# Kernel optimization log

Measured on AMD Instinct MI355X. Metric: run time of the kernel, lower is better.

The kernel has to match this reference:

```python
import jax, jax.numpy as jnp
import numpy as np

DIM = 768
HEADS = 12
HEAD_DIM = DIM // HEADS
SCALE = HEAD_DIM ** -0.5
B = 8
N = 2121   # 1 cls + 1600 + 400 + 100 + 20 text
NT = 20

# token ranges: cls [0,1), x0 [1,1601), x1 [1601,2001), x2 [2001,2101), t [2101,2121)
SLICES = {'cls': (0, 1), 'x0': (1, 1601), 'x1': (1601, 2001), 'x2': (2001, 2101), 't': (2101, 2121)}


def setup_inputs() -> dict:
    key = jax.random.key(0)
    k1, k2, k3, k4 = jax.random.split(key, 4)
    src = jax.random.normal(k1, (B, N, DIM), dtype=jnp.float32)
    visu_mask = jnp.zeros((B, 2101), dtype=bool)   # True = masked out
    text_mask = jnp.zeros((B, NT), dtype=bool)
    w_qkv = jax.random.normal(k2, (DIM, 3 * DIM), dtype=jnp.float32) * 0.02
    w_proj = jax.random.normal(k3, (DIM, DIM), dtype=jnp.float32) * 0.02
    b_proj = jax.random.normal(k4, (DIM,), dtype=jnp.float32) * 0.02
    return {'src': src, 'visu_mask': visu_mask, 'text_mask': text_mask,
            'w_qkv': w_qkv, 'w_proj': w_proj, 'b_proj': b_proj}


def _attn(q, k, v, mask):
    # q: [B,H,Nq,D], k/v: [B,H,Nk,D], mask: [B,Nk] bool (True = masked)
    scores = jnp.einsum('bhqd,bhkd->bhqk', q * SCALE, k)
    scores = jnp.where(mask[:, None, None, :], -jnp.inf, scores)
    p = jax.nn.softmax(scores, axis=-1)
    o = jnp.einsum('bhqk,bhkd->bhqd', p, v)          # [B,H,Nq,D]
    return o.transpose(0, 2, 1, 3).reshape(q.shape[0], q.shape[2], -1)  # [B,Nq,C]


def reference(src, visu_mask, text_mask, w_qkv, w_proj, b_proj):
    qkv = (src @ w_qkv).reshape(B, N, 3, HEADS, HEAD_DIM).transpose(2, 0, 3, 1, 4)
    q, k, v = qkv[0], qkv[1], qkv[2]                  # [B,H,N,D]

    def blk(t, lo, hi):
        return t[:, :, lo:hi, :]

    (c0, c1), (a0, a1), (b0, b1), (d0, d1), (t0, t1) = (
        SLICES['cls'], SLICES['x0'], SLICES['x1'], SLICES['x2'], SLICES['t'])

    x0_mask = visu_mask[:, a0:a1]
    x1_mask = visu_mask[:, b0:b1]
    x2_mask = visu_mask[:, d0:d1]
    full_mask = jnp.concatenate([visu_mask, text_mask], axis=1)   # [B, N]

    # cls attends to everything
    cls = _attn(blk(q, c0, c1), k, v, full_mask)
    # x2 attends to x0+x1+x2+t
    k_x2 = jnp.concatenate([blk(k, a0, a1), blk(k, b0, b1), blk(k, d0, d1), blk(k, t0, t1)], axis=2)
    v_x2 = jnp.concatenate([blk(v, a0, a1), blk(v, b0, b1), blk(v, d0, d1), blk(v, t0, t1)], axis=2)
    m_x2 = jnp.concatenate([x0_mask, x1_mask, x2_mask, text_mask], axis=1)
    x2 = _attn(blk(q, d0, d1), k_x2, v_x2, m_x2)
    # x1 attends to x0+x1+t
    k_x1 = jnp.concatenate([blk(k, a0, a1), blk(k, b0, b1), blk(k, t0, t1)], axis=2)
    v_x1 = jnp.concatenate([blk(v, a0, a1), blk(v, b0, b1), blk(v, t0, t1)], axis=2)
    m_x1 = jnp.concatenate([x0_mask, x1_mask, text_mask], axis=1)
    x1 = _attn(blk(q, b0, b1), k_x1, v_x1, m_x1)
    # x0 attends to x0+t
    k_x0 = jnp.concatenate([blk(k, a0, a1), blk(k, t0, t1)], axis=2)
    v_x0 = jnp.concatenate([blk(v, a0, a1), blk(v, t0, t1)], axis=2)
    m_x0 = jnp.concatenate([x0_mask, text_mask], axis=1)
    x0 = _attn(blk(q, a0, a1), k_x0, v_x0, m_x0)
    # text attends to everything
    t = _attn(blk(q, t0, t1), k, v, full_mask)

    x = jnp.concatenate([cls, x0, x1, x2, t], axis=1)
    return x @ w_proj + b_proj
```

## Files before the change

### kernel.cpp

```cpp
#include <hip/hip_runtime.h>
#include <stdint.h>

typedef short           bf16x8 __attribute__((ext_vector_type(8)));
typedef float           f32x4  __attribute__((ext_vector_type(4)));
typedef float           f32x16 __attribute__((ext_vector_type(16)));
typedef unsigned short  u16;
typedef u16             u16x8  __attribute__((ext_vector_type(8)));
typedef uint32_t        u32;

#define NB    8
#define NSEQ  2121
#define NPAD  2176
#define MROWS 16968
#define MPAD  17024
#define NH    12

#if __has_builtin(__builtin_amdgcn_exp2f)
#define EXP2F(x) __builtin_amdgcn_exp2f(x)
#else
#define EXP2F(x) exp2f(x)
#endif

#define MASK_BIAS   (-30000.0f)
#define INVALID_S   (-90000.0f)

__device__ __forceinline__ u16 f2bf(float f) {
  uint32_t u = __float_as_uint(f);
  u += 0x7fffu + ((u >> 16) & 1u);
  return (u16)(u >> 16);
}

__global__ void transpose_cast(const float* __restrict__ in, u16* __restrict__ out,
                               int R, int C, int scale_cols, float scale)
{
  __shared__ float tile[32][33];
  const int c0 = blockIdx.x * 32, r0 = blockIdx.y * 32;
  const int tx = threadIdx.x, ty = threadIdx.y;
#pragma unroll
  for (int i = 0; i < 4; i++) {
    const int r = r0 + ty + i * 8;
    tile[ty + i * 8][tx] = in[(size_t)r * C + c0 + tx];
  }
  __syncthreads();
#pragma unroll
  for (int i = 0; i < 4; i++) {
    const int c = c0 + ty + i * 8;
    float v = tile[tx][ty + i * 8];
    if (c < scale_cols) v *= scale;
    out[(size_t)c * R + r0 + tx] = f2bf(v);
  }
}

__global__ __launch_bounds__(256) void gemm_qkv_kernel(
    const float* __restrict__ src, const u16* __restrict__ wt,
    u16* __restrict__ qk, u16* __restrict__ vt)
{
  __shared__ u16 As[128][40];
  __shared__ u16 Bs[128][40];
  const int tid  = threadIdx.x;
  const int lane = tid & 63, wave = tid >> 6;
  const int wr = wave >> 1, wc = wave & 1;
  const int col = lane & 15, grp = lane >> 4;
  const int m0 = blockIdx.y * 128, n0 = blockIdx.x * 128;
  const int arow = tid >> 1, akoff = (tid & 1) * 16;

  const f32x4 fz = {0.f, 0.f, 0.f, 0.f};
  f32x4 acc[4][4];
#pragma unroll
  for (int i = 0; i < 4; i++)
#pragma unroll
    for (int j = 0; j < 4; j++) acc[i][j] = fz;

  const int m = m0 + arow;
  const bool mv = m < MROWS;
  const float4* sbase = (const float4*)(src + (size_t)m * 768 + akoff);
  const u16*   bbase  = wt + (size_t)(n0 + arow) * 768 + akoff;

  float4 a0 = {0,0,0,0}, a1 = {0,0,0,0}, a2 = {0,0,0,0}, a3 = {0,0,0,0};
  u16x8 bb0, bb1;
  if (mv) { a0 = sbase[0]; a1 = sbase[1]; a2 = sbase[2]; a3 = sbase[3]; }
  bb0 = *(const u16x8*)(bbase);
  bb1 = *(const u16x8*)(bbase + 8);

  for (int kb = 0; kb < 768; kb += 32) {
    u16x8 t0, t1;
    t0[0] = f2bf(a0.x); t0[1] = f2bf(a0.y); t0[2] = f2bf(a0.z); t0[3] = f2bf(a0.w);
    t0[4] = f2bf(a1.x); t0[5] = f2bf(a1.y); t0[6] = f2bf(a1.z); t0[7] = f2bf(a1.w);
    t1[0] = f2bf(a2.x); t1[1] = f2bf(a2.y); t1[2] = f2bf(a2.z); t1[3] = f2bf(a2.w);
    t1[4] = f2bf(a3.x); t1[5] = f2bf(a3.y); t1[6] = f2bf(a3.z); t1[7] = f2bf(a3.w);
    *(u16x8*)&As[arow][akoff]     = t0;
    *(u16x8*)&As[arow][akoff + 8] = t1;
    *(u16x8*)&Bs[arow][akoff]     = bb0;
    *(u16x8*)&Bs[arow][akoff + 8] = bb1;
    __syncthreads();

    if (kb + 32 < 768) {
      const int o = (kb + 32) >> 2;
      if (mv) { a0 = sbase[o]; a1 = sbase[o + 1]; a2 = sbase[o + 2]; a3 = sbase[o + 3]; }
      bb0 = *(const u16x8*)(bbase + kb + 32);
      bb1 = *(const u16x8*)(bbase + kb + 40);
    }

    bf16x8 af[4], bfr[4];
#pragma unroll
    for (int mt = 0; mt < 4; mt++) af[mt]  = *(const bf16x8*)&As[wr * 64 + mt * 16 + col][grp * 8];
#pragma unroll
    for (int nt = 0; nt < 4; nt++) bfr[nt] = *(const bf16x8*)&Bs[wc * 64 + nt * 16 + col][grp * 8];
#pragma unroll
    for (int mt = 0; mt < 4; mt++)
#pragma unroll
      for (int nt = 0; nt < 4; nt++)
        acc[mt][nt] = __builtin_amdgcn_mfma_f32_16x16x32_bf16(af[mt], bfr[nt], acc[mt][nt], 0, 0, 0);
    __syncthreads();
  }

#pragma unroll
  for (int mt = 0; mt < 4; mt++) {
#pragma unroll
    for (int r = 0; r < 4; r++) {
      const int mm = m0 + wr * 64 + mt * 16 + grp * 4 + r;
      if (mm >= MROWS) continue;
      const uint32_t bb = (uint32_t)mm / 2121u;
      const uint32_t nn = (uint32_t)mm - bb * 2121u;
#pragma unroll
      for (int nt = 0; nt < 4; nt++) {
        const int c = n0 + wc * 64 + nt * 16 + col;
        const u16 bits = f2bf(acc[mt][nt][r]);
        if (c < 1536) {
          qk[(size_t)mm * 1536 + c] = bits;
        } else {
          const int hd = c - 1536;
          const int h = hd >> 6, d = hd & 63;
          vt[((size_t)(bb * NH + h) * 64 + d) * NPAD + nn] = bits;
        }
      }
    }
  }
}

__global__ __launch_bounds__(256) void gemm_proj_kernel(
    const u16* __restrict__ A, const u16* __restrict__ Bt,
    const float* __restrict__ bias, float* __restrict__ out)
{
  __shared__ u16 As[128][40];
  __shared__ u16 Bs[128][40];
  const int tid  = threadIdx.x;
  const int lane = tid & 63, wave = tid >> 6;
  const int wr = wave >> 1, wc = wave & 1;
  const int col = lane & 15, grp = lane >> 4;
  const int m0 = blockIdx.y * 128, n0 = blockIdx.x * 128;
  const int arow = tid >> 1, akoff = (tid & 1) * 16;

  const f32x4 fz = {0.f, 0.f, 0.f, 0.f};
  f32x4 acc[4][4];
#pragma unroll
  for (int i = 0; i < 4; i++)
#pragma unroll
    for (int j = 0; j < 4; j++) acc[i][j] = fz;

  const u16* abase = A  + (size_t)(m0 + arow) * 768 + akoff;
  const u16* bbase = Bt + (size_t)(n0 + arow) * 768 + akoff;
  u16x8 aa0, aa1, bb0, bb1;
  aa0 = *(const u16x8*)(abase);
  aa1 = *(const u16x8*)(abase + 8);
  bb0 = *(const u16x8*)(bbase);
  bb1 = *(const u16x8*)(bbase + 8);

  for (int kb = 0; kb < 768; kb += 32) {
    *(u16x8*)&As[arow][akoff]     = aa0;
    *(u16x8*)&As[arow][akoff + 8] = aa1;
    *(u16x8*)&Bs[arow][akoff]     = bb0;
    *(u16x8*)&Bs[arow][akoff + 8] = bb1;
    __syncthreads();

    if (kb + 32 < 768) {
      aa0 = *(const u16x8*)(abase + kb + 32);
      aa1 = *(const u16x8*)(abase + kb + 40);
      bb0 = *(const u16x8*)(bbase + kb + 32);
      bb1 = *(const u16x8*)(bbase + kb + 40);
    }

    bf16x8 af[4], bfr[4];
#pragma unroll
    for (int mt = 0; mt < 4; mt++) af[mt]  = *(const bf16x8*)&As[wr * 64 + mt * 16 + col][grp * 8];
#pragma unroll
    for (int nt = 0; nt < 4; nt++) bfr[nt] = *(const bf16x8*)&Bs[wc * 64 + nt * 16 + col][grp * 8];
#pragma unroll
    for (int mt = 0; mt < 4; mt++)
#pragma unroll
      for (int nt = 0; nt < 4; nt++)
        acc[mt][nt] = __builtin_amdgcn_mfma_f32_16x16x32_bf16(af[mt], bfr[nt], acc[mt][nt], 0, 0, 0);
    __syncthreads();
  }

#pragma unroll
  for (int mt = 0; mt < 4; mt++) {
#pragma unroll
    for (int r = 0; r < 4; r++) {
      const int mm = m0 + wr * 64 + mt * 16 + grp * 4 + r;
      if (mm >= MROWS) continue;
#pragma unroll
      for (int nt = 0; nt < 4; nt++) {
        const int c = n0 + wc * 64 + nt * 16 + col;
        out[(size_t)mm * 768 + c] = acc[mt][nt][r] + bias[c];
      }
    }
  }
}

__global__ __launch_bounds__(256) void attn_kernel(
    const u16* __restrict__ qkbuf, const u16* __restrict__ vt,
    const unsigned char* __restrict__ visu, const unsigned char* __restrict__ text,
    u16* __restrict__ attnout)
{
  __shared__ __align__(16) u16 Ks[2][64][72];
  __shared__ __align__(16) u16 Vs[2][64][72];
  __shared__ __align__(16) float biasAll[NPAD];
  __shared__ __align__(16) float lduf[4][32];
  __shared__ u32 tileflags[34];

  const int tid  = threadIdx.x;
  const int lane = tid & 63, wave = tid >> 6;
  const int l31 = lane & 31, h = lane >> 5;

  const int fid = blockIdx.x;
  const int swz = (fid & 7) * 204 + (fid >> 3);
  const int qtile = swz % 17;
  const int bh = swz / 17;
  const int b = bh / NH, hh = bh % NH;
  const int qt0 = qtile * 128;
  const int q0 = qt0 + wave * 32;
  const int qrow = q0 + l31;

  for (int i = tid; i < NPAD; i += 256) {
    float bb = MASK_BIAS;
    if (i < 2101)      bb = visu[b * 2101 + i] ? MASK_BIAS : 0.0f;
    else if (i < 2121) bb = text[b * 20 + (i - 2101)] ? MASK_BIAS : 0.0f;
    biasAll[i] = bb;
  }
  if (tid < 34) tileflags[tid] = 0u;
  __syncthreads();
  if (tid < 136) {
    const int t = tid >> 2;
    const float* p = &biasAll[t * 64 + (tid & 3) * 16];
    float s = 0.f;
#pragma unroll
    for (int j = 0; j < 16; j++) s += p[j];
    if (s != 0.f) atomicOr(&tileflags[t], 1u);
  }

  bf16x8 qf[4];
  {
    const u16* qp = qkbuf + (size_t)(b * NSEQ + qrow) * 1536 + hh * 64 + h * 8;
#pragma unroll
    for (int s = 0; s < 4; s++) qf[s] = *(const bf16x8*)(qp + s * 16);
  }

  int ks, ke, ex;
  if (qrow == 0)        { ks = 0; ke = 2121; ex = 0; }
  else if (qrow < 1601) { ks = 1; ke = 1601; ex = 1; }
  else if (qrow < 2001) { ks = 1; ke = 2001; ex = 1; }
  else if (qrow < 2101) { ks = 1; ke = 2121; ex = 0; }
  else if (qrow < 2121) { ks = 0; ke = 2121; ex = 0; }
  else                  { ks = 0; ke = 0;    ex = 0; }

  const int hi = (qt0 + 127 < 2120) ? (qt0 + 127) : 2120;
  int ke_tile, extra;
  if (qt0 == 0 || hi >= 2001) { ke_tile = 2121; extra = 0; }
  else if (hi >= 1601)        { ke_tile = 2001; extra = 1; }
  else                        { ke_tile = 1601; extra = 1; }
  const int nkv = (ke_tile + 63) >> 6;
  const int ntot = nkv + extra;

  f32x16 O0, O1;
#pragma unroll
  for (int i = 0; i < 16; i++) { O0[i] = 0.f; O1[i] = 0.f; }
  float lrun = 0.f;

  const int srow = tid >> 2, skoff = (tid & 3) * 16;
  const size_t vbase = (size_t)(b * NH + hh) * 64 * NPAD;
  const u16* kbase = qkbuf + (size_t)(b * NSEQ + srow) * 1536 + 768 + hh * 64 + skoff;
  const u16* vrow  = vt + vbase + (size_t)srow * NPAD + skoff;

  {
    u16x8 k0 = *(const u16x8*)kbase;
    u16x8 k1 = *(const u16x8*)(kbase + 8);
    u16x8 v0 = *(const u16x8*)vrow;
    u16x8 v1 = *(const u16x8*)(vrow + 8);
    *(u16x8*)&Ks[0][srow][skoff]     = k0;
    *(u16x8*)&Ks[0][srow][skoff + 8] = k1;
    *(u16x8*)&Vs[0][srow][skoff]     = v0;
    *(u16x8*)&Vs[0][srow][skoff + 8] = v1;
  }
  __syncthreads();

  u16x8 kpre0, kpre1, vpre0, vpre1;

  for (int it = 0; it < ntot; ++it) {
    const int cur = it & 1;
    const int kv0 = (it < nkv) ? it * 64 : 2096;
    const bool more = (it + 1 < ntot);

    if (more) {
      const int kvn = (it + 1 < nkv) ? (it + 1) * 64 : 2096;
      const u16* kp = kbase + (size_t)kvn * 1536;
      kpre0 = *(const u16x8*)kp;
      kpre1 = *(const u16x8*)(kp + 8);
      const u16* vp = vrow + kvn;
      vpre0 = *(const u16x8*)vp;
      vpre1 = *(const u16x8*)(vp + 8);
    }

    const int skipl = (kv0 >= ke) && !((ex != 0) && (kv0 < 2121) && (kv0 + 64 > 2101));
    if (!__all(skipl)) {
      f32x16 S0, S1;
#pragma unroll
      for (int i = 0; i < 16; i++) { S0[i] = 0.f; S1[i] = 0.f; }
      __builtin_amdgcn_s_setprio(1);
#pragma unroll
      for (int s = 0; s < 4; s++) {
        const bf16x8 k0 = *(const bf16x8*)&Ks[cur][l31][s * 16 + h * 8];
        const bf16x8 k1 = *(const bf16x8*)&Ks[cur][32 + l31][s * 16 + h * 8];
        S0 = __builtin_amdgcn_mfma_f32_32x32x16_bf16(k0, qf[s], S0, 0, 0, 0);
        S1 = __builtin_amdgcn_mfma_f32_32x32x16_bf16(k1, qf[s], S1, 0, 0, 0);
      }
      __builtin_amdgcn_s_setprio(0);

      const int fastl = (kv0 >= ks) && (kv0 + 64 <= ke);
      const bool tf = (it < nkv) ? (tileflags[it] != 0u) : true;
      const bool plain = __all(fastl) && !tf;
      if (!plain) {
#pragma unroll
        for (int m = 0; m < 4; m++) {
          const f32x4 b0 = *(const f32x4*)&biasAll[kv0 + 8 * m + 4 * h];
          const f32x4 b1 = *(const f32x4*)&biasAll[kv0 + 32 + 8 * m + 4 * h];
#pragma unroll
          for (int r = 0; r < 4; r++) {
            {
              const int key = kv0 + 8 * m + 4 * h + r;
              const bool valid = ((key >= ks) && (key < ke)) ||
                                 ((ex != 0) && (key >= 2101) && (key < 2121));
              const float sv = S0[4 * m + r] + b0[r];
              S0[4 * m + r] = valid ? sv : INVALID_S;
            }
            {
              const int key = kv0 + 32 + 8 * m + 4 * h + r;
              const bool valid = ((key >= ks) && (key < ke)) ||
                                 ((ex != 0) && (key >= 2101) && (key < 2121));
              const float sv = S1[4 * m + r] + b1[r];
              S1[4 * m + r] = valid ? sv : INVALID_S;
            }
          }
        }
      }

      float ls = 0.f;
#pragma unroll
      for (int i = 0; i < 16; i++) { const float p = EXP2F(S0[i]); S0[i] = p; ls += p; }
#pragma unroll
      for (int i = 0; i < 16; i++) { const float p = EXP2F(S1[i]); S1[i] = p; ls += p; }
      lrun += ls;

      bf16x8 pa[4];
      {
        u32 w[8];
#pragma unroll
        for (int j = 0; j < 8; j++) {
          u32 t;
          asm("v_cvt_pk_bf16_f32 %0, %1, %2" : "=v"(t) : "v"(S0[2 * j]), "v"(S0[2 * j + 1]));
          w[j] = t;
        }
        asm("v_permlane32_swap_b32 %0, %1" : "+v"(w[0]), "+v"(w[2]));
        asm("v_permlane32_swap_b32 %0, %1" : "+v"(w[1]), "+v"(w[3]));
        asm("v_permlane32_swap_b32 %0, %1" : "+v"(w[4]), "+v"(w[6]));
        asm("v_permlane32_swap_b32 %0, %1" : "+v"(w[5]), "+v"(w[7]));
        union { u32 u[4]; bf16x8 v; } f0, f1;
        f0.u[0] = w[0]; f0.u[1] = w[1]; f0.u[2] = w[2]; f0.u[3] = w[3];
        f1.u[0] = w[4]; f1.u[1] = w[5]; f1.u[2] = w[6]; f1.u[3] = w[7];
        pa[0] = f0.v; pa[1] = f1.v;
      }
      {
        u32 w[8];
#pragma unroll
        for (int j = 0; j < 8; j++) {
          u32 t;
          asm("v_cvt_pk_bf16_f32 %0, %1, %2" : "=v"(t) : "v"(S1[2 * j]), "v"(S1[2 * j + 1]));
          w[j] = t;
        }
        asm("v_permlane32_swap_b32 %0, %1" : "+v"(w[0]), "+v"(w[2]));
        asm("v_permlane32_swap_b32 %0, %1" : "+v"(w[1]), "+v"(w[3]));
        asm("v_permlane32_swap_b32 %0, %1" : "+v"(w[4]), "+v"(w[6]));
        asm("v_permlane32_swap_b32 %0, %1" : "+v"(w[5]), "+v"(w[7]));
        union { u32 u[4]; bf16x8 v; } f0, f1;
        f0.u[0] = w[0]; f0.u[1] = w[1]; f0.u[2] = w[2]; f0.u[3] = w[3];
        f1.u[0] = w[4]; f1.u[1] = w[5]; f1.u[2] = w[6]; f1.u[3] = w[7];
        pa[2] = f0.v; pa[3] = f1.v;
      }

      __builtin_amdgcn_s_setprio(1);
#pragma unroll
      for (int ck = 0; ck < 4; ck++) {
        const bf16x8 vf0 = *(const bf16x8*)&Vs[cur][l31][ck * 16 + h * 8];
        const bf16x8 vf1 = *(const bf16x8*)&Vs[cur][32 + l31][ck * 16 + h * 8];
        O0 = __builtin_amdgcn_mfma_f32_32x32x16_bf16(pa[ck], vf0, O0, 0, 0, 0);
        O1 = __builtin_amdgcn_mfma_f32_32x32x16_bf16(pa[ck], vf1, O1, 0, 0, 0);
      }
      __builtin_amdgcn_s_setprio(0);
    }

    if (more) {
      *(u16x8*)&Ks[cur ^ 1][srow][skoff]     = kpre0;
      *(u16x8*)&Ks[cur ^ 1][srow][skoff + 8] = kpre1;
      *(u16x8*)&Vs[cur ^ 1][srow][skoff]     = vpre0;
      *(u16x8*)&Vs[cur ^ 1][srow][skoff + 8] = vpre1;
    }
    __syncthreads();
  }

  float ltot = lrun + __shfl_xor(lrun, 32);
  if (h == 0) lduf[wave][l31] = ltot;
#pragma unroll
  for (int m = 0; m < 4; m++) {
    const f32x4 lv = *(const f32x4*)&lduf[wave][8 * m + 4 * h];
#pragma unroll
    for (int r = 0; r < 4; r++) {
      const float linv = (lv[r] > 0.f) ? 1.0f / lv[r] : 0.f;
      const int n = q0 + 8 * m + 4 * h + r;
      if (n >= NSEQ) continue;
      u16* op = attnout + (size_t)(b * NSEQ + n) * 768 + hh * 64 + l31;
      op[0]  = f2bf(O0[4 * m + r] * linv);
      op[32] = f2bf(O1[4 * m + r] * linv);
    }
  }
}

extern "C" void kernel_launch(void* const* d_in, const int* in_sizes, int n_in,
                              void* d_out, int out_size, void* d_ws, size_t ws_size,
                              hipStream_t stream) {
  const float* src  = (const float*)d_in[0];
  const unsigned char* visu = (const unsigned char*)d_in[1];
  const unsigned char* text = (const unsigned char*)d_in[2];
  const float* w_qkv = (const float*)d_in[3];
  const float* w_proj = (const float*)d_in[4];
  const float* b_proj = (const float*)d_in[5];
  float* out = (float*)d_out;

  char* ws = (char*)d_ws;
  size_t off = 0;
  auto alloc = [&](size_t bytes) { char* p = ws + off; off += (bytes + 255) & ~(size_t)255; return p; };
  u16* wqkv_t  = (u16*)alloc((size_t)2304 * 768 * 2);
  u16* wproj_t = (u16*)alloc((size_t)768 * 768 * 2);
  u16* qk      = (u16*)alloc((size_t)MPAD * 1536 * 2);
  u16* vtb     = (u16*)alloc((size_t)NB * NH * 64 * NPAD * 2);
  u16* attnb   = (u16*)alloc((size_t)MPAD * 768 * 2);
  (void)ws_size; (void)in_sizes; (void)n_in; (void)out_size;

  transpose_cast<<<dim3(2304 / 32, 768 / 32), dim3(32, 8), 0, stream>>>(w_qkv, wqkv_t, 768, 2304, 768, 0.125f * 1.4426950408889634f);
  transpose_cast<<<dim3(768 / 32, 768 / 32), dim3(32, 8), 0, stream>>>(w_proj, wproj_t, 768, 768, 0, 1.0f);
  gemm_qkv_kernel<<<dim3(18, 133), dim3(256), 0, stream>>>(src, wqkv_t, qk, vtb);
  attn_kernel<<<dim3(1632), dim3(256), 0, stream>>>(qk, vtb, visu, text, attnb);
  gemm_proj_kernel<<<dim3(6, 133), dim3(256), 0, stream>>>(attnb, wproj_t, b_proj, out);
}
```

Before: 408.7 us.

## Precast src to bf16, widen attention tiles to 256 queries, bitmask key masks

A separate kernel casts src to bf16 once, so the QKV GEMM loads bf16 directly instead of converting fp32 inside the K loop. The attention kernel goes to 512 threads with 256-query tiles, so each K/V tile loaded into shared memory is reused by twice as many query rows. The per-key float bias array and tile flags are replaced by 64-bit ballot bitmasks, and the bf16 src buffer is reused as the attention output. The extra cast kernel adds a full read and write of src, and the larger blocks cut the grid from 1632 to 864 blocks, which may reduce occupancy and load balance.

Result: faster. 391.8 us (-4.1%).

```diff
diff --git a/kernel.cpp b/kernel.cpp
--- a/kernel.cpp
+++ b/kernel.cpp
@@ -7,6 +7,7 @@
 typedef unsigned short  u16;
 typedef u16             u16x8  __attribute__((ext_vector_type(8)));
 typedef uint32_t        u32;
+typedef unsigned long long u64;
 
 #define NB    8
 #define NSEQ  2121
@@ -21,7 +22,6 @@
 #define EXP2F(x) exp2f(x)
 #endif
 
-#define MASK_BIAS   (-30000.0f)
 #define INVALID_S   (-90000.0f)
 
 __device__ __forceinline__ u16 f2bf(float f) {
@@ -51,8 +51,20 @@
   }
 }
 
+__global__ __launch_bounds__(256) void cast_src_bf16(const float* __restrict__ in,
+                                                     u16* __restrict__ out)
+{
+  const size_t i = ((size_t)blockIdx.x * 256 + threadIdx.x) * 8;
+  float4 a = *(const float4*)(in + i);
+  float4 b = *(const float4*)(in + i + 4);
+  u16x8 t;
+  t[0] = f2bf(a.x); t[1] = f2bf(a.y); t[2] = f2bf(a.z); t[3] = f2bf(a.w);
+  t[4] = f2bf(b.x); t[5] = f2bf(b.y); t[6] = f2bf(b.z); t[7] = f2bf(b.w);
+  *(u16x8*)(out + i) = t;
+}
+
 __global__ __launch_bounds__(256) void gemm_qkv_kernel(
-    const float* __restrict__ src, const u16* __restrict__ wt,
+    const u16* __restrict__ srcb, const u16* __restrict__ wt,
     u16* __restrict__ qk, u16* __restrict__ vt)
 {
   __shared__ u16 As[128][40];
@@ -71,32 +83,24 @@
 #pragma unroll
     for (int j = 0; j < 4; j++) acc[i][j] = fz;
 
-  const int m = m0 + arow;
-  const bool mv = m < MROWS;
-  const float4* sbase = (const float4*)(src + (size_t)m * 768 + akoff);
-  const u16*   bbase  = wt + (size_t)(n0 + arow) * 768 + akoff;
-
-  float4 a0 = {0,0,0,0}, a1 = {0,0,0,0}, a2 = {0,0,0,0}, a3 = {0,0,0,0};
-  u16x8 bb0, bb1;
-  if (mv) { a0 = sbase[0]; a1 = sbase[1]; a2 = sbase[2]; a3 = sbase[3]; }
+  const u16* abase = srcb + (size_t)(m0 + arow) * 768 + akoff;
+  const u16* bbase = wt   + (size_t)(n0 + arow) * 768 + akoff;
+  u16x8 aa0, aa1, bb0, bb1;
+  aa0 = *(const u16x8*)(abase);
+  aa1 = *(const u16x8*)(abase + 8);
   bb0 = *(const u16x8*)(bbase);
   bb1 = *(const u16x8*)(bbase + 8);
 
   for (int kb = 0; kb < 768; kb += 32) {
-    u16x8 t0, t1;
-    t0[0] = f2bf(a0.x); t0[1] = f2bf(a0.y); t0[2] = f2bf(a0.z); t0[3] = f2bf(a0.w);
-    t0[4] = f2bf(a1.x); t0[5] = f2bf(a1.y); t0[6] = f2bf(a1.z); t0[7] = f2bf(a1.w);
-    t1[0] = f2bf(a2.x); t1[1] = f2bf(a2.y); t1[2] = f2bf(a2.z); t1[3] = f2bf(a2.w);
-    t1[4] = f2bf(a3.x); t1[5] = f2bf(a3.y); t1[6] = f2bf(a3.z); t1[7] = f2bf(a3.w);
-    *(u16x8*)&As[arow][akoff]     = t0;
-    *(u16x8*)&As[arow][akoff + 8] = t1;
+    *(u16x8*)&As[arow][akoff]     = aa0;
+    *(u16x8*)&As[arow][akoff + 8] = aa1;
     *(u16x8*)&Bs[arow][akoff]     = bb0;
     *(u16x8*)&Bs[arow][akoff + 8] = bb1;
     __syncthreads();
 
     if (kb + 32 < 768) {
-      const int o = (kb + 32) >> 2;
-      if (mv) { a0 = sbase[o]; a1 = sbase[o + 1]; a2 = sbase[o + 2]; a3 = sbase[o + 3]; }
+      aa0 = *(const u16x8*)(abase + kb + 32);
+      aa1 = *(const u16x8*)(abase + kb + 40);
       bb0 = *(const u16x8*)(bbase + kb + 32);
       bb1 = *(const u16x8*)(bbase + kb + 40);
     }
@@ -208,50 +212,42 @@
   }
 }
 
-__global__ __launch_bounds__(256) void attn_kernel(
+__global__ __launch_bounds__(512) void attn_kernel(
     const u16* __restrict__ qkbuf, const u16* __restrict__ vt,
     const unsigned char* __restrict__ visu, const unsigned char* __restrict__ text,
     u16* __restrict__ attnout)
 {
   __shared__ __align__(16) u16 Ks[2][64][72];
   __shared__ __align__(16) u16 Vs[2][64][72];
-  __shared__ __align__(16) float biasAll[NPAD];
-  __shared__ __align__(16) float lduf[4][32];
-  __shared__ u32 tileflags[34];
+  __shared__ __align__(16) u64 mb64[34];
+  __shared__ __align__(16) float lduf[8][32];
 
   const int tid  = threadIdx.x;
   const int lane = tid & 63, wave = tid >> 6;
   const int l31 = lane & 31, h = lane >> 5;
 
   const int fid = blockIdx.x;
-  const int swz = (fid & 7) * 204 + (fid >> 3);
-  const int qtile = swz % 17;
-  const int bh = swz / 17;
+  const int swz = (fid & 7) * 108 + (fid >> 3);
+  const int qtile = swz % 9;
+  const int bh = swz / 9;
   const int b = bh / NH, hh = bh % NH;
-  const int qt0 = qtile * 128;
+  const int qt0 = qtile * 256;
   const int q0 = qt0 + wave * 32;
   const int qrow = q0 + l31;
 
-  for (int i = tid; i < NPAD; i += 256) {
-    float bb = MASK_BIAS;
-    if (i < 2101)      bb = visu[b * 2101 + i] ? MASK_BIAS : 0.0f;
-    else if (i < 2121) bb = text[b * 20 + (i - 2101)] ? MASK_BIAS : 0.0f;
-    biasAll[i] = bb;
-  }
-  if (tid < 34) tileflags[tid] = 0u;
-  __syncthreads();
-  if (tid < 136) {
-    const int t = tid >> 2;
-    const float* p = &biasAll[t * 64 + (tid & 3) * 16];
-    float s = 0.f;
-#pragma unroll
-    for (int j = 0; j < 16; j++) s += p[j];
-    if (s != 0.f) atomicOr(&tileflags[t], 1u);
-  }
-
+  for (int c = wave; c < 34; c += 8) {
+    const int key = c * 64 + lane;
+    int mb = 1;
+    if (key < 2101)      mb = visu[b * 2101 + key] ? 1 : 0;
+    else if (key < 2121) mb = text[b * 20 + (key - 2101)] ? 1 : 0;
+    const u64 bal = __ballot(mb != 0);
+    if (lane == 0) mb64[c] = bal;
+  }
+
+  const int qload = (qrow < NSEQ) ? qrow : (NSEQ - 1);
   bf16x8 qf[4];
   {
-    const u16* qp = qkbuf + (size_t)(b * NSEQ + qrow) * 1536 + hh * 64 + h * 8;
+    const u16* qp = qkbuf + (size_t)(b * NSEQ + qload) * 1536 + hh * 64 + h * 8;
 #pragma unroll
     for (int s = 0; s < 4; s++) qf[s] = *(const bf16x8*)(qp + s * 16);
   }
@@ -264,7 +260,7 @@
   else if (qrow < 2121) { ks = 0; ke = 2121; ex = 0; }
   else                  { ks = 0; ke = 0;    ex = 0; }
 
-  const int hi = (qt0 + 127 < 2120) ? (qt0 + 127) : 2120;
+  const int hi = (qt0 + 255 < 2120) ? (qt0 + 255) : 2120;
   int ke_tile, extra;
   if (qt0 == 0 || hi >= 2001) { ke_tile = 2121; extra = 0; }
   else if (hi >= 1601)        { ke_tile = 2001; extra = 1; }
@@ -277,24 +273,16 @@
   for (int i = 0; i < 16; i++) { O0[i] = 0.f; O1[i] = 0.f; }
   float lrun = 0.f;
 
-  const int srow = tid >> 2, skoff = (tid & 3) * 16;
+  const int srow = tid >> 3, skoff = (tid & 7) * 8;
   const size_t vbase = (size_t)(b * NH + hh) * 64 * NPAD;
   const u16* kbase = qkbuf + (size_t)(b * NSEQ + srow) * 1536 + 768 + hh * 64 + skoff;
   const u16* vrow  = vt + vbase + (size_t)srow * NPAD + skoff;
 
-  {
-    u16x8 k0 = *(const u16x8*)kbase;
-    u16x8 k1 = *(const u16x8*)(kbase + 8);
-    u16x8 v0 = *(const u16x8*)vrow;
-    u16x8 v1 = *(const u16x8*)(vrow + 8);
-    *(u16x8*)&Ks[0][srow][skoff]     = k0;
-    *(u16x8*)&Ks[0][srow][skoff + 8] = k1;
-    *(u16x8*)&Vs[0][srow][skoff]     = v0;
-    *(u16x8*)&Vs[0][srow][skoff + 8] = v1;
-  }
+  *(u16x8*)&Ks[0][srow][skoff] = *(const u16x8*)kbase;
+  *(u16x8*)&Vs[0][srow][skoff] = *(const u16x8*)vrow;
   __syncthreads();
 
-  u16x8 kpre0, kpre1, vpre0, vpre1;
+  u16x8 kpre, vpre;
 
   for (int it = 0; it < ntot; ++it) {
     const int cur = it & 1;
@@ -303,12 +291,8 @@
 
     if (more) {
       const int kvn = (it + 1 < nkv) ? (it + 1) * 64 : 2096;
-      const u16* kp = kbase + (size_t)kvn * 1536;
-      kpre0 = *(const u16x8*)kp;
-      kpre1 = *(const u16x8*)(kp + 8);
-      const u16* vp = vrow + kvn;
-      vpre0 = *(const u16x8*)vp;
-      vpre1 = *(const u16x8*)(vp + 8);
+      kpre = *(const u16x8*)(kbase + (size_t)kvn * 1536);
+      vpre = *(const u16x8*)(vrow + kvn);
     }
 
     const int skipl = (kv0 >= ke) && !((ex != 0) && (kv0 < 2121) && (kv0 + 64 > 2101));
@@ -327,28 +311,26 @@
       __builtin_amdgcn_s_setprio(0);
 
       const int fastl = (kv0 >= ks) && (kv0 + 64 <= ke);
-      const bool tf = (it < nkv) ? (tileflags[it] != 0u) : true;
-      const bool plain = __all(fastl) && !tf;
+      const u64 mword = (it < nkv) ? mb64[it] : ((mb64[32] >> 48) | (mb64[33] << 16));
+      const bool plain = __all(fastl) && (mword == 0ull);
       if (!plain) {
+        const u32 wlo = (u32)mword, whi = (u32)(mword >> 32);
 #pragma unroll
         for (int m = 0; m < 4; m++) {
-          const f32x4 b0 = *(const f32x4*)&biasAll[kv0 + 8 * m + 4 * h];
-          const f32x4 b1 = *(const f32x4*)&biasAll[kv0 + 32 + 8 * m + 4 * h];
 #pragma unroll
           for (int r = 0; r < 4; r++) {
+            const int bitpos = 8 * m + 4 * h + r;
             {
-              const int key = kv0 + 8 * m + 4 * h + r;
-              const bool valid = ((key >= ks) && (key < ke)) ||
-                                 ((ex != 0) && (key >= 2101) && (key < 2121));
-              const float sv = S0[4 * m + r] + b0[r];
-              S0[4 * m + r] = valid ? sv : INVALID_S;
+              const int key = kv0 + bitpos;
+              bool valid = ((key >= ks) && (key < ke)) || ((ex != 0) && (key >= 2101));
+              valid = valid && (((wlo >> bitpos) & 1u) == 0u);
+              S0[4 * m + r] = valid ? S0[4 * m + r] : INVALID_S;
             }
             {
-              const int key = kv0 + 32 + 8 * m + 4 * h + r;
-              const bool valid = ((key >= ks) && (key < ke)) ||
-                                 ((ex != 0) && (key >= 2101) && (key < 2121));
-              const float sv = S1[4 * m + r] + b1[r];
-              S1[4 * m + r] = valid ? sv : INVALID_S;
+              const int key = kv0 + 32 + bitpos;
+              bool valid = ((key >= ks) && (key < ke)) || ((ex != 0) && (key >= 2101));
+              valid = valid && (((whi >> bitpos) & 1u) == 0u);
+              S1[4 * m + r] = valid ? S1[4 * m + r] : INVALID_S;
             }
           }
         }
@@ -409,10 +391,8 @@
     }
 
     if (more) {
-      *(u16x8*)&Ks[cur ^ 1][srow][skoff]     = kpre0;
-      *(u16x8*)&Ks[cur ^ 1][srow][skoff + 8] = kpre1;
-      *(u16x8*)&Vs[cur ^ 1][srow][skoff]     = vpre0;
-      *(u16x8*)&Vs[cur ^ 1][srow][skoff + 8] = vpre1;
+      *(u16x8*)&Ks[cur ^ 1][srow][skoff] = kpre;
+      *(u16x8*)&Vs[cur ^ 1][srow][skoff] = vpre;
     }
     __syncthreads();
   }
@@ -452,12 +432,13 @@
   u16* wproj_t = (u16*)alloc((size_t)768 * 768 * 2);
   u16* qk      = (u16*)alloc((size_t)MPAD * 1536 * 2);
   u16* vtb     = (u16*)alloc((size_t)NB * NH * 64 * NPAD * 2);
-  u16* attnb   = (u16*)alloc((size_t)MPAD * 768 * 2);
+  u16* tmp0    = (u16*)alloc((size_t)MPAD * 768 * 2);
   (void)ws_size; (void)in_sizes; (void)n_in; (void)out_size;
 
   transpose_cast<<<dim3(2304 / 32, 768 / 32), dim3(32, 8), 0, stream>>>(w_qkv, wqkv_t, 768, 2304, 768, 0.125f * 1.4426950408889634f);
   transpose_cast<<<dim3(768 / 32, 768 / 32), dim3(32, 8), 0, stream>>>(w_proj, wproj_t, 768, 768, 0, 1.0f);
-  gemm_qkv_kernel<<<dim3(18, 133), dim3(256), 0, stream>>>(src, wqkv_t, qk, vtb);
-  attn_kernel<<<dim3(1632), dim3(256), 0, stream>>>(qk, vtb, visu, text, attnb);
-  gemm_proj_kernel<<<dim3(6, 133), dim3(256), 0, stream>>>(attnb, wproj_t, b_proj, out);
-}
+  cast_src_bf16<<<dim3(6363), dim3(256), 0, stream>>>(src, tmp0);
+  gemm_qkv_kernel<<<dim3(18, 133), dim3(256), 0, stream>>>(tmp0, wqkv_t, qk, vtb);
+  attn_kernel<<<dim3(864), dim3(512), 0, stream>>>(qk, vtb, visu, text, tmp0);
+  gemm_proj_kernel<<<dim3(6, 133), dim3(256), 0, stream>>>(tmp0, wproj_t, b_proj, out);
+}
```
